# Kernel optimization log

Hardware: AMD Instinct MI355X
Metric: run time of the kernel (lower is better)

The kernel has to match this reference:

```python
import jax, jax.numpy as jnp
import numpy as np

EMB = 1024
B, N = 4, 2048


def setup_inputs() -> dict:
    key = jax.random.key(0)
    ks = jax.random.split(key, 10)
    s = 1.0 / np.sqrt(EMB)
    return {
        "x": jax.random.normal(ks[0], (B, N, EMB), dtype=jnp.float32),
        "Wq": jax.random.normal(ks[1], (EMB, EMB), dtype=jnp.float32) * s,
        "bq": jnp.zeros((EMB,), dtype=jnp.float32),
        "Wk": jax.random.normal(ks[2], (EMB, EMB), dtype=jnp.float32) * s,
        "bk": jnp.zeros((EMB,), dtype=jnp.float32),
        "Wv": jax.random.normal(ks[3], (EMB, EMB), dtype=jnp.float32) * s,
        "bv": jnp.zeros((EMB,), dtype=jnp.float32),
        "Wm": jax.random.normal(ks[4], (EMB, EMB), dtype=jnp.float32) * s,
        "bm": jnp.zeros((EMB,), dtype=jnp.float32),
    }


def reference(x, Wq, bq, Wk, bk, Wv, bv, Wm, bm):
    # Projections (torch Linear: x @ W^T + b; here W is stored pre-transposed)
    q = x @ Wq + bq  # [B,N,D]
    k = x @ Wk + bk
    v = x @ Wv + bv
    # scores[b,i,j] = q[b,i,:] . k[b,j,:]  (no 1/sqrt(d) scaling in original)
    scores = jnp.einsum("bid,bjd->bij", q, k)
    # NOTE: softmax over dim=1 (the query/i axis), as in the original
    alpha = jax.nn.softmax(scores, axis=1)  # [B,N,N]
    # t[b,j,d] = sum_i v[b,i,d] * alpha[b,i,j]  == alpha^T @ v per batch
    t = jnp.einsum("bij,bid->bjd", alpha, v)  # [B,N,D]
    # MLP(emb, emb, []) is a single Linear, followed by outer relu
    return jax.nn.relu(t @ Wm + bm)
```

## Files before the change

### kernel.cpp

```cpp
#include <hip/hip_runtime.h>
#include <hip/hip_bf16.h>
#include <hip/hip_fp16.h>
#include <math.h>

#define EMB 1024
#define SEQ 2048
#define BATCH 4

typedef _Float16 half8 __attribute__((ext_vector_type(8)));
typedef float floatx4 __attribute__((ext_vector_type(4)));

__device__ __forceinline__ void gload_lds16(const void* g, void* l) {
    __builtin_amdgcn_global_load_lds(
        (const __attribute__((address_space(1))) void*)g,
        (__attribute__((address_space(3))) void*)l, 16, 0, 0);
}

template <int EPI>
__global__ __launch_bounds__(256) void gemm_bt(
    const _Float16* __restrict__ A, const _Float16* __restrict__ B,
    void* __restrict__ Cv, const float* __restrict__ bias,
    int M, int N, int K, long sAb, long sBb, long sCb) {
    __shared__ _Float16 As[128 * 64];
    __shared__ _Float16 Bs[128 * 64];
    const int tid = threadIdx.x;
    const int lane = tid & 63;
    const int wave = tid >> 6;
    const long zb = blockIdx.z;
    A += zb * sAb;
    B += zb * sBb;
    const int bm = blockIdx.x * 128;
    const int bn = blockIdx.y * 128;
    floatx4 acc[4][4];
#pragma unroll
    for (int mi = 0; mi < 4; ++mi)
#pragma unroll
        for (int ni = 0; ni < 4; ++ni) acc[mi][ni] = (floatx4){0.f, 0.f, 0.f, 0.f};

    const int row_in = lane >> 3;
    const int col_in = (lane & 7) * 8;
    const int wm = (wave >> 1) * 64;
    const int wn = (wave & 1) * 64;
    const int fr = lane & 15;
    const int fk = (lane >> 4) * 8;

    for (int kt = 0; kt < K; kt += 64) {
#pragma unroll
        for (int c = 0; c < 4; ++c) {
            const int cc = wave * 4 + c;
            const _Float16* ga = A + (long)(bm + cc * 8 + row_in) * K + kt + col_in;
            gload_lds16(ga, &As[cc * 512]);
            const _Float16* gb = B + (long)(bn + cc * 8 + row_in) * K + kt + col_in;
            gload_lds16(gb, &Bs[cc * 512]);
        }
        __syncthreads();
#pragma unroll
        for (int kk = 0; kk < 64; kk += 32) {
            half8 af[4], bf[4];
#pragma unroll
            for (int mi = 0; mi < 4; ++mi)
                af[mi] = *(const half8*)&As[(wm + mi * 16 + fr) * 64 + kk + fk];
#pragma unroll
            for (int ni = 0; ni < 4; ++ni)
                bf[ni] = *(const half8*)&Bs[(wn + ni * 16 + fr) * 64 + kk + fk];
#pragma unroll
            for (int mi = 0; mi < 4; ++mi)
#pragma unroll
                for (int ni = 0; ni < 4; ++ni)
                    acc[mi][ni] = __builtin_amdgcn_mfma_f32_16x16x32_f16(
                        af[mi], bf[ni], acc[mi][ni], 0, 0, 0);
        }
        __syncthreads();
    }

    const int er = (lane >> 4) * 4;
    const int ec = lane & 15;
#pragma unroll
    for (int mi = 0; mi < 4; ++mi) {
#pragma unroll
        for (int ni = 0; ni < 4; ++ni) {
            const int col = bn + wn + ni * 16 + ec;
#pragma unroll
            for (int r = 0; r < 4; ++r) {
                const int row = bm + wm + mi * 16 + er + r;
                float v = acc[mi][ni][r];
                if (EPI == 0 || EPI == 1 || EPI == 3) v += bias[col];
                if (EPI == 3) v = fmaxf(v, 0.f);
                if (EPI == 0 || EPI == 4) {
                    ((_Float16*)Cv)[zb * sCb + (long)row * N + col] = (_Float16)v;
                } else if (EPI == 1) {
                    const long b = row >> 11;
                    const long i = row & (SEQ - 1);
                    ((_Float16*)Cv)[(b * EMB + col) * SEQ + i] = (_Float16)v;
                } else {
                    ((float*)Cv)[zb * sCb + (long)row * N + col] = v;
                }
            }
        }
    }
}

__global__ __launch_bounds__(256) void softmax_rows(const float* __restrict__ P,
                                                    _Float16* __restrict__ Aout) {
    const long row = blockIdx.x;
    const float* p = P + row * (long)SEQ;
    const int tid = threadIdx.x;
    float4 x0 = ((const float4*)p)[2 * tid];
    float4 x1 = ((const float4*)p)[2 * tid + 1];
    float v[8] = {x0.x, x0.y, x0.z, x0.w, x1.x, x1.y, x1.z, x1.w};
    float m = v[0];
#pragma unroll
    for (int j = 1; j < 8; ++j) m = fmaxf(m, v[j]);
#pragma unroll
    for (int o = 32; o; o >>= 1) m = fmaxf(m, __shfl_xor(m, o));
    __shared__ float rbuf[4];
    __shared__ float sbuf[4];
    const int lane = tid & 63, wv = tid >> 6;
    if (!lane) rbuf[wv] = m;
    __syncthreads();
    m = fmaxf(fmaxf(rbuf[0], rbuf[1]), fmaxf(rbuf[2], rbuf[3]));
    float s = 0.f;
#pragma unroll
    for (int j = 0; j < 8; ++j) {
        v[j] = expf(v[j] - m);
        s += v[j];
    }
#pragma unroll
    for (int o = 32; o; o >>= 1) s += __shfl_xor(s, o);
    if (!lane) sbuf[wv] = s;
    __syncthreads();
    s = sbuf[0] + sbuf[1] + sbuf[2] + sbuf[3];
    const float inv = 1.f / s;
    half8 h;
#pragma unroll
    for (int j = 0; j < 8; ++j) h[j] = (_Float16)(v[j] * inv);
    *(half8*)(Aout + row * (long)SEQ + tid * 8) = h;
}

__global__ __launch_bounds__(256) void cast_x(const float* __restrict__ X,
                                              _Float16* __restrict__ Xh) {
    const long i = (long)(blockIdx.x * 256 + threadIdx.x) * 8;
    float4 a = ((const float4*)(X + i))[0];
    float4 b = ((const float4*)(X + i))[1];
    half8 h;
    h[0] = (_Float16)a.x; h[1] = (_Float16)a.y; h[2] = (_Float16)a.z; h[3] = (_Float16)a.w;
    h[4] = (_Float16)b.x; h[5] = (_Float16)b.y; h[6] = (_Float16)b.z; h[7] = (_Float16)b.w;
    *(half8*)(Xh + i) = h;
}

__global__ __launch_bounds__(256) void transpose_cast(const float* __restrict__ W,
                                                      _Float16* __restrict__ Wt) {
    __shared__ float tile[32][33];
    const int bx = blockIdx.x * 32;
    const int by = blockIdx.y * 32;
    const int tx = threadIdx.x, ty = threadIdx.y;
#pragma unroll
    for (int r = 0; r < 32; r += 8)
        tile[ty + r][tx] = W[(long)(by + ty + r) * EMB + bx + tx];
    __syncthreads();
#pragma unroll
    for (int r = 0; r < 32; r += 8)
        Wt[(long)(bx + ty + r) * EMB + by + tx] = (_Float16)tile[tx][ty + r];
}

extern "C" void kernel_launch(void* const* d_in, const int* in_sizes, int n_in,
                              void* d_out, int out_size, void* d_ws, size_t ws_size,
                              hipStream_t stream) {
    const float* x  = (const float*)d_in[0];
    const float* Wq = (const float*)d_in[1];
    const float* bq = (const float*)d_in[2];
    const float* Wk = (const float*)d_in[3];
    const float* bk = (const float*)d_in[4];
    const float* Wv = (const float*)d_in[5];
    const float* bv = (const float*)d_in[6];
    const float* Wm = (const float*)d_in[7];
    const float* bm = (const float*)d_in[8];
    float* out = (float*)d_out;

    char* ws = (char*)d_ws;
    const long MB = 1l << 20;
    _Float16* xh  = (_Float16*)(ws + 0 * MB);
    _Float16* wqt = (_Float16*)(ws + 16 * MB);
    _Float16* wkt = (_Float16*)(ws + 18 * MB);
    _Float16* wvt = (_Float16*)(ws + 20 * MB);
    _Float16* wmt = (_Float16*)(ws + 22 * MB);
    _Float16* q   = (_Float16*)(ws + 24 * MB);
    _Float16* k   = (_Float16*)(ws + 40 * MB);
    _Float16* vt  = (_Float16*)(ws + 56 * MB);
    _Float16* t   = (_Float16*)(ws + 72 * MB);
    float*    P   = (float*)(ws + 88 * MB);
    _Float16* al  = (_Float16*)(ws + 152 * MB);

    const long MN = (long)BATCH * SEQ;

    cast_x<<<4096, 256, 0, stream>>>(x, xh);
    transpose_cast<<<dim3(32, 32), dim3(32, 8), 0, stream>>>(Wq, wqt);
    transpose_cast<<<dim3(32, 32), dim3(32, 8), 0, stream>>>(Wk, wkt);
    transpose_cast<<<dim3(32, 32), dim3(32, 8), 0, stream>>>(Wv, wvt);
    transpose_cast<<<dim3(32, 32), dim3(32, 8), 0, stream>>>(Wm, wmt);

    gemm_bt<0><<<dim3(64, 8), 256, 0, stream>>>(xh, wqt, q, bq, (int)MN, EMB, EMB, 0, 0, 0);
    gemm_bt<0><<<dim3(64, 8), 256, 0, stream>>>(xh, wkt, k, bk, (int)MN, EMB, EMB, 0, 0, 0);
    gemm_bt<1><<<dim3(64, 8), 256, 0, stream>>>(xh, wvt, vt, bv, (int)MN, EMB, EMB, 0, 0, 0);

    gemm_bt<2><<<dim3(16, 16, BATCH), 256, 0, stream>>>(
        k, q, P, nullptr, SEQ, SEQ, EMB,
        (long)SEQ * EMB, (long)SEQ * EMB, (long)SEQ * SEQ);

    softmax_rows<<<BATCH * SEQ, 256, 0, stream>>>(P, al);

    gemm_bt<4><<<dim3(16, 8, BATCH), 256, 0, stream>>>(
        al, vt, t, nullptr, SEQ, EMB, SEQ,
        (long)SEQ * SEQ, (long)EMB * SEQ, (long)SEQ * EMB);

    gemm_bt<3><<<dim3(64, 8), 256, 0, stream>>>(t, wmt, out, bm, (int)MN, EMB, EMB, 0, 0, 0);
}
```

Baseline: 345.3 us.

## Double-buffer LDS tiles in GEMM to overlap global loads with MFMA

Replaces the single 64-wide K tile with two 32-wide LDS buffers in a ping-pong pipeline. The next tile is prefetched via global_load_lds while MFMAs run on the current one, with an explicit vmcnt wait plus barrier between stages. This aims to hide global memory latency behind compute. In exchange, each iteration does half the K work per barrier, so there are twice as many barriers.

After: 350.9 us. About the same (+1.6%).

```diff
diff --git a/kernel.cpp b/kernel.cpp
--- a/kernel.cpp
+++ b/kernel.cpp
@@ -14,6 +14,12 @@
     __builtin_amdgcn_global_load_lds(
         (const __attribute__((address_space(1))) void*)g,
         (__attribute__((address_space(3))) void*)l, 16, 0, 0);
+}
+
+__device__ __forceinline__ void pipe_sync() {
+    asm volatile("s_waitcnt vmcnt(0)" ::: "memory");
+    __builtin_amdgcn_s_barrier();
+    __builtin_amdgcn_sched_barrier(0);
 }
 
 template <int EPI>
@@ -21,8 +27,10 @@
     const _Float16* __restrict__ A, const _Float16* __restrict__ B,
     void* __restrict__ Cv, const float* __restrict__ bias,
     int M, int N, int K, long sAb, long sBb, long sCb) {
-    __shared__ _Float16 As[128 * 64];
-    __shared__ _Float16 Bs[128 * 64];
+    __shared__ _Float16 As0[128 * 32];
+    __shared__ _Float16 Bs0[128 * 32];
+    __shared__ _Float16 As1[128 * 32];
+    __shared__ _Float16 Bs1[128 * 32];
     const int tid = threadIdx.x;
     const int lane = tid & 63;
     const int wave = tid >> 6;
@@ -37,41 +45,50 @@
 #pragma unroll
         for (int ni = 0; ni < 4; ++ni) acc[mi][ni] = (floatx4){0.f, 0.f, 0.f, 0.f};
 
-    const int row_in = lane >> 3;
-    const int col_in = (lane & 7) * 8;
+    const int srow = lane >> 2;
+    const int scol = (lane & 3) * 8;
     const int wm = (wave >> 1) * 64;
     const int wn = (wave & 1) * 64;
     const int fr = lane & 15;
     const int fk = (lane >> 4) * 8;
 
-    for (int kt = 0; kt < K; kt += 64) {
-#pragma unroll
-        for (int c = 0; c < 4; ++c) {
-            const int cc = wave * 4 + c;
-            const _Float16* ga = A + (long)(bm + cc * 8 + row_in) * K + kt + col_in;
-            gload_lds16(ga, &As[cc * 512]);
-            const _Float16* gb = B + (long)(bn + cc * 8 + row_in) * K + kt + col_in;
-            gload_lds16(gb, &Bs[cc * 512]);
-        }
-        __syncthreads();
-#pragma unroll
-        for (int kk = 0; kk < 64; kk += 32) {
-            half8 af[4], bf[4];
-#pragma unroll
-            for (int mi = 0; mi < 4; ++mi)
-                af[mi] = *(const half8*)&As[(wm + mi * 16 + fr) * 64 + kk + fk];
-#pragma unroll
-            for (int ni = 0; ni < 4; ++ni)
-                bf[ni] = *(const half8*)&Bs[(wn + ni * 16 + fr) * 64 + kk + fk];
-#pragma unroll
-            for (int mi = 0; mi < 4; ++mi)
-#pragma unroll
-                for (int ni = 0; ni < 4; ++ni)
-                    acc[mi][ni] = __builtin_amdgcn_mfma_f32_16x16x32_f16(
-                        af[mi], bf[ni], acc[mi][ni], 0, 0, 0);
-        }
-        __syncthreads();
-    }
+#define STAGE(AS, BS, kt)                                                      \
+    {                                                                          \
+        _Pragma("unroll") for (int c = 0; c < 2; ++c) {                        \
+            const int rr = wave * 32 + c * 16 + srow;                          \
+            gload_lds16(A + (long)(bm + rr) * K + (kt) + scol,                 \
+                        &AS[(wave * 2 + c) * 512]);                            \
+            gload_lds16(B + (long)(bn + rr) * K + (kt) + scol,                 \
+                        &BS[(wave * 2 + c) * 512]);                            \
+        }                                                                      \
+    }
+
+#define COMPUTE(AS, BS)                                                        \
+    {                                                                          \
+        half8 af[4], bf[4];                                                    \
+        _Pragma("unroll") for (int mi = 0; mi < 4; ++mi)                       \
+            af[mi] = *(const half8*)&AS[(wm + mi * 16 + fr) * 32 + fk];        \
+        _Pragma("unroll") for (int ni = 0; ni < 4; ++ni)                       \
+            bf[ni] = *(const half8*)&BS[(wn + ni * 16 + fr) * 32 + fk];        \
+        _Pragma("unroll") for (int mi = 0; mi < 4; ++mi)                       \
+            _Pragma("unroll") for (int ni = 0; ni < 4; ++ni)                   \
+                acc[mi][ni] = __builtin_amdgcn_mfma_f32_16x16x32_f16(          \
+                    af[mi], bf[ni], acc[mi][ni], 0, 0, 0);                     \
+    }
+
+    const int T = K >> 5;
+    STAGE(As0, Bs0, 0);
+    pipe_sync();
+    for (int t = 0; t < T; t += 2) {
+        STAGE(As1, Bs1, (t + 1) << 5);
+        COMPUTE(As0, Bs0);
+        pipe_sync();
+        if (t + 2 < T) STAGE(As0, Bs0, (t + 2) << 5);
+        COMPUTE(As1, Bs1);
+        pipe_sync();
+    }
+#undef STAGE
+#undef COMPUTE
 
     const int er = (lane >> 4) * 4;
     const int ec = lane & 15;
```
